# Performance work log

Hardware: AMD Instinct MI355X
Metric: run time of the kernel (lower is better)

Reference implementation:

```python
import jax, jax.numpy as jnp
import numpy as np

V_IN, V_OUT = 32000, 32000
E, H = 512, 1024
B, S, T = 64, 128, 64


def setup_inputs() -> dict:
    key = jax.random.key(0)
    ks = jax.random.split(key, 13)
    s = 0.05
    return {
        "src": jax.random.randint(ks[0], (B, S), 0, V_IN, dtype=jnp.int32),
        "trg": jax.random.randint(ks[1], (B, T), 0, V_OUT, dtype=jnp.int32),
        "tf_mask": jax.random.randint(ks[2], (T,), 0, 2, dtype=jnp.int32),
        "enc_emb": jax.random.normal(ks[3], (V_IN, E), jnp.float32) * s,
        "dec_emb": jax.random.normal(ks[4], (V_OUT, E), jnp.float32) * s,
        "Wih_e": jax.random.normal(ks[5], (4 * H, E), jnp.float32) * s,
        "Whh_e": jax.random.normal(ks[6], (4 * H, H), jnp.float32) * s,
        "b_e": jax.random.normal(ks[7], (4 * H,), jnp.float32) * s,
        "Wih_d": jax.random.normal(ks[8], (4 * H, E), jnp.float32) * s,
        "Whh_d": jax.random.normal(ks[9], (4 * H, H), jnp.float32) * s,
        "b_d": jax.random.normal(ks[10], (4 * H,), jnp.float32) * s,
        "Wfc": jax.random.normal(ks[11], (V_OUT, H), jnp.float32) * s,
        "bfc": jax.random.normal(ks[12], (V_OUT,), jnp.float32) * s,
    }


def lstm_step(h, c, x, Wih, Whh, b):
    # PyTorch LSTM gate order: input, forget, cell(g), output
    g = x @ Wih.T + h @ Whh.T + b  # [B, 4H]
    i, f, gg, o = jnp.split(g, 4, axis=-1)
    c_new = jax.nn.sigmoid(f) * c + jax.nn.sigmoid(i) * jnp.tanh(gg)
    h_new = jax.nn.sigmoid(o) * jnp.tanh(c_new)
    return h_new, c_new


def reference(src, trg, tf_mask, enc_emb, dec_emb, Wih_e, Whh_e, b_e,
              Wih_d, Whh_d, b_d, Wfc, bfc):
    b, t_len = trg.shape
    dt = Wfc.dtype
    hdim = Whh_e.shape[1]

    # ----- Encoder (dropout is identity in eval mode) -----
    x_src = enc_emb[src]  # [B, S, E]
    h0 = jnp.zeros((b, hdim), dt)
    c0 = jnp.zeros((b, hdim), dt)

    def enc_step(carry, x_t):
        h, c = carry
        h, c = lstm_step(h, c, x_t, Wih_e, Whh_e, b_e)
        return (h, c), None

    (h, c), _ = jax.lax.scan(enc_step, (h0, c0), jnp.swapaxes(x_src, 0, 1))

    # ----- Decoder loop over t = 1 .. T-1 -----
    def dec_step(carry, xs):
        h, c, inp = carry
        trg_t, tf = xs
        x = dec_emb[inp]  # [B, E]
        h, c = lstm_step(h, c, x, Wih_d, Whh_d, b_d)
        logits = h @ Wfc.T + bfc  # [B, V]
        nxt = jnp.where(tf > 0, trg_t, jnp.argmax(logits, axis=-1).astype(trg_t.dtype))
        return (h, c, nxt), logits

    xs = (jnp.swapaxes(trg, 0, 1)[1:], tf_mask[1:])
    _, logits = jax.lax.scan(dec_step, (h, c, trg[:, 0]), xs)  # [T-1, B, V]

    # outputs[:, 0, :] stays zeros, as in the original
    out = jnp.concatenate([jnp.zeros((1, b, logits.shape[-1]), logits.dtype), logits], axis=0)
    return jnp.swapaxes(out, 0, 1)  # [B, T, V]
```

## Files before the change

### kernel.cpp

```cpp
#include <hip/hip_runtime.h>
#include <math.h>

#define Hd 1024
#define Ed 512
#define Bv 64
#define Sv 128
#define Tv 64
#define Vv 32000
#define NB 256

typedef __attribute__((ext_vector_type(8))) short bf16x8;
typedef __attribute__((ext_vector_type(4))) float f32x4;
typedef unsigned long long ull;

__device__ __forceinline__ float sigf(float x){ return 1.0f/(1.0f + expf(-x)); }
__device__ __forceinline__ unsigned short f2bf(float f){
  unsigned u = __float_as_uint(f);
  return (unsigned short)((u + 0x7FFFu + ((u>>16)&1u)) >> 16);
}
__device__ __forceinline__ float bf2f(unsigned short b){ return __uint_as_float(((unsigned)b)<<16); }
__device__ __forceinline__ void split3(float v, unsigned short& s0, unsigned short& s1, unsigned short& s2){
  s0 = f2bf(v);
  float r1 = v - bf2f(s0);
  s1 = f2bf(r1);
  s2 = f2bf(r1 - bf2f(s1));
}
#define MF(A,B,C) __builtin_amdgcn_mfma_f32_16x16x32_bf16(A,B,C,0,0,0)

#define OFF_H    65536
#define H_PL     4259840L
#define OFF_WE   6455296
#define OFF_WD   15892480
#define W_PL     6291456L
#define OFF_WF   25329664
#define WF_PL    32768000L
#define OFF_TOK  58097664
#define OFF_CNT  58105728
#define NEED_FL  58106240


__global__ __launch_bounds__(256) void k_wsplit3(
    const float* __restrict__ Wih, const float* __restrict__ Whh,
    unsigned short* __restrict__ d0, unsigned short* __restrict__ d1, unsigned short* __restrict__ d2)
{
  const int n = blockIdx.x;
  const int tid = threadIdx.x;
  const int g = n >> 10, jt = (n & 1023) >> 4, nl = n & 15;
  const long base = ((long)(g*64 + jt)*48) << 9;
  #pragma unroll
  for (int i = 0; i < 6; ++i){
    int k = tid + 256*i;
    float v = (k < 512) ? Wih[(long)n*512 + k] : Whh[(long)n*1024 + (k-512)];
    int kt = k >> 5, lk = (k >> 3) & 3, ke = k & 7;
    long dst = base + ((long)kt << 9) + ((lk*16 + nl) << 3) + ke;
    unsigned short s0,s1,s2; split3(v, s0,s1,s2);
    d0[dst] = s0; d1[dst] = s1; d2[dst] = s2;
  }
}

__global__ __launch_bounds__(256) void k_wfsplit(
    const float* __restrict__ W, unsigned short* __restrict__ dhi, unsigned short* __restrict__ dlo)
{
  const int v = blockIdx.x;
  const int tid = threadIdx.x;
  const int vt = v >> 4, vl = v & 15;
  const long base = ((long)vt*32) << 9;
  #pragma unroll
  for (int i = 0; i < 4; ++i){
    int k = tid + 256*i;
    float x = W[(long)v*1024 + k];
    int kt = k >> 5, lk = (k >> 3) & 3, ke = k & 7;
    long dst = base + ((long)kt << 9) + ((lk*16 + vl) << 3) + ke;
    unsigned short h = f2bf(x);
    dhi[dst] = h;
    dlo[dst] = f2bf(x - bf2f(h));
  }
}

__device__ __forceinline__ void gbar(int* cnt, int idx){
  __syncthreads();
  if (threadIdx.x == 0){
    __hip_atomic_fetch_add(&cnt[idx], 1, __ATOMIC_RELEASE, __HIP_MEMORY_SCOPE_AGENT);
    while (__hip_atomic_load(&cnt[idx], __ATOMIC_RELAXED, __HIP_MEMORY_SCOPE_AGENT) < NB)
      __builtin_amdgcn_s_sleep(2);
    __builtin_amdgcn_fence(__ATOMIC_ACQUIRE, "workgroup");
  }
  __syncthreads();
}

template<bool DEC>
__device__ __forceinline__ void lstm_phase(
    int lb, int tid, int slot_in, int slot_out, int tj,
    const unsigned short* __restrict__ W0s, const unsigned short* __restrict__ W1s,
    const unsigned short* __restrict__ W2s, const float* __restrict__ bias,
    const int* __restrict__ tok_src, const int* __restrict__ tf,
    const float* __restrict__ emb, const ull* __restrict__ toku,
    unsigned short* __restrict__ H, float* __restrict__ c,
    float (*g4)[16][16], short (*hst)[16][16], int* stok)
{
  const bool act = (tid < 256);
  const int g = (tid >> 6) & 3, lane = tid & 63;
  const int l15 = lane & 15, lk = lane >> 4;
  const int jh = (lb & 63) * 16;
  const int m0 = (lb >> 6) * 16;
  const int mt = lb >> 6;
  const long wbase = ((long)(g*64 + (lb & 63))*48) << 9;
  const unsigned short* w0 = W0s + wbase;
  const unsigned short* w1 = W1s + wbase;
  const unsigned short* w2 = W2s + wbase;
  const unsigned short* h0 = H + (long)slot_in*65536;
  const unsigned short* h1 = h0 + H_PL;
  const unsigned short* h2 = h0 + 2*H_PL;

  if (tid < 16){
    int m = m0 + tid, tk;
    if (!DEC){
      tk = tok_src[m*Sv + tj];
    } else {
      if (tj == 0) tk = tok_src[m*Tv];
      else if (tf[tj] > 0) tk = tok_src[m*Tv + tj];
      else tk = (int)(~(unsigned)__hip_atomic_load(&toku[(long)(tj-1)*64 + m],
                     __ATOMIC_RELAXED, __HIP_MEMORY_SCOPE_AGENT));
    }
    stok[tid] = tk;
  }
  __syncthreads();

  if (act){
    f32x4 acc = (f32x4){0.f,0.f,0.f,0.f};

    {
      const float* e0 = emb + (long)stok[l15]*Ed;
      #pragma unroll 2
      for (int kt = 0; kt < 16; ++kt){
        const int k0 = kt*32 + lk*8;
        bf16x8 b0  = *(const bf16x8*)(w0 + ((long)kt << 9) + (lane << 3));
        bf16x8 b1v = *(const bf16x8*)(w1 + ((long)kt << 9) + (lane << 3));
        bf16x8 b2  = *(const bf16x8*)(w2 + ((long)kt << 9) + (lane << 3));
        bf16x8 a0,a1,a2;
        float4 pa = *(const float4*)(e0 + k0);
        float4 pb = *(const float4*)(e0 + k0 + 4);
        float fv[8] = {pa.x,pa.y,pa.z,pa.w,pb.x,pb.y,pb.z,pb.w};
        #pragma unroll
        for (int e=0;e<8;++e){ unsigned short s0,s1,s2; split3(fv[e],s0,s1,s2);
          a0[e]=(short)s0; a1[e]=(short)s1; a2[e]=(short)s2; }
        acc = MF(a0,b0,acc); acc = MF(a1,b0,acc); acc = MF(a0,b1v,acc);
        acc = MF(a2,b0,acc); acc = MF(a0,b2,acc); acc = MF(a1,b1v,acc);
      }
    }
    {
      #pragma unroll 2
      for (int kt = 0; kt < 32; ++kt){
        bf16x8 b0  = *(const bf16x8*)(w0 + ((long)(16+kt) << 9) + (lane << 3));
        bf16x8 b1v = *(const bf16x8*)(w1 + ((long)(16+kt) << 9) + (lane << 3));
        bf16x8 b2  = *(const bf16x8*)(w2 + ((long)(16+kt) << 9) + (lane << 3));
        const long ho = (((long)mt*32 + kt) << 9) + (lane << 3);
        bf16x8 a0 = *(const bf16x8*)(h0 + ho);
        bf16x8 a1 = *(const bf16x8*)(h1 + ho);
        bf16x8 a2 = *(const bf16x8*)(h2 + ho);
        acc = MF(a0,b0,acc); acc = MF(a1,b0,acc); acc = MF(a0,b1v,acc);
        acc = MF(a2,b0,acc); acc = MF(a0,b2,acc); acc = MF(a1,b1v,acc);
      }
    }

    #pragma unroll
    for (int r = 0; r < 4; ++r) g4[g][lk*4 + r][l15] = acc[r];
  }
  __syncthreads();

  if (act){
    const int mloc = tid >> 4, cl = tid & 15;
    const int col = jh + cl;
    float ig = g4[0][mloc][cl] + bias[col];
    float fg = g4[1][mloc][cl] + bias[Hd + col];
    float gg = g4[2][mloc][cl] + bias[2*Hd + col];
    float og = g4[3][mloc][cl] + bias[3*Hd + col];
    long idx = (long)(m0 + mloc)*Hd + col;
    float cv = c[idx];
    float cn = sigf(fg)*cv + sigf(ig)*tanhf(gg);
    float hn = sigf(og)*tanhf(cn);
    c[idx] = cn;
    unsigned short s0,s1,s2; split3(hn, s0,s1,s2);
    hst[0][mloc][cl] = (short)s0; hst[1][mloc][cl] = (short)s1; hst[2][mloc][cl] = (short)s2;
  }
  __syncthreads();
  if (tid < 192){
    const int p = tid >> 6, t2 = tid & 63, r = t2 >> 2, q = t2 & 3;
    ull v =
        (ull)(unsigned short)hst[p][r][q*4]
      | ((ull)(unsigned short)hst[p][r][q*4+1] << 16)
      | ((ull)(unsigned short)hst[p][r][q*4+2] << 32)
      | ((ull)(unsigned short)hst[p][r][q*4+3] << 48);
    const int kt = (lb & 63) >> 1;
    const int off16 = (jh & 16) + q*4;
    const int lkw = off16 >> 3, keb = off16 & 7;
    ull* dst = (ull*)(H + (long)p*H_PL + (long)slot_out*65536
                      + (((long)mt*32 + kt) << 9) + ((lkw*16 + r) << 3) + keb);
    __hip_atomic_store(dst, v, __ATOMIC_RELAXED, __HIP_MEMORY_SCOPE_AGENT);
  }
}

__device__ __forceinline__ void fc_phase(
    int b, int tid,
    const unsigned short* __restrict__ hhi, const unsigned short* __restrict__ hlo,
    const unsigned short* __restrict__ Wfhi, const unsigned short* __restrict__ Wflo,
    const float* __restrict__ bfc,
    ull* __restrict__ tslot, ull* amax)
{
  if (tid < 64) amax[tid] = 0ULL;
  __syncthreads();
  const int wv = tid >> 6, lane = tid & 63;
  const int l15 = lane & 15, lk = lane >> 4;
  const int vt = b*8 + wv;
  const int v0 = vt*16 + l15;

  f32x4 acc[4];
  #pragma unroll
  for (int mt=0; mt<4; ++mt) acc[mt] = (f32x4){0.f,0.f,0.f,0.f};

  #pragma unroll 2
  for (int kt = 0; kt < 32; ++kt){
    const long wo = (((long)vt*32 + kt) << 9) + (lane << 3);
    bf16x8 bh = *(const bf16x8*)(Wfhi + wo);
    bf16x8 bl = *(const bf16x8*)(Wflo + wo);
    #pragma unroll
    for (int mt=0; mt<4; ++mt){
      const long ho = (((long)mt*32 + kt) << 9) + (lane << 3);
      bf16x8 ah = *(const bf16x8*)(hhi + ho);
      bf16x8 al = *(const bf16x8*)(hlo + ho);
      acc[mt] = MF(ah, bh, acc[mt]);
      acc[mt] = MF(al, bh, acc[mt]);
      acc[mt] = MF(ah, bl, acc[mt]);
    }
  }
  float bb0 = bfc[v0];
  #pragma unroll
  for (int mt=0; mt<4; ++mt){
    #pragma unroll
    for (int r=0; r<4; ++r){
      int m = mt*16 + lk*4 + r;
      float f0 = acc[mt][r] + bb0;
      unsigned u0 = __float_as_uint(f0); u0 ^= (u0 >> 31) ? 0xFFFFFFFFu : 0x80000000u;
      ull cm = ((ull)u0 << 32) | (unsigned)(~v0);
      #pragma unroll
      for (int d=1; d<16; d<<=1){
        ull o = __shfl_xor(cm, d);
        if (o > cm) cm = o;
      }
      if (l15 == 0) atomicMax(&amax[m], cm);
    }
  }
  __syncthreads();
  if (tid < 64) atomicMax(tslot + tid, amax[tid]);
}

__global__ __launch_bounds__(512, 1) void k_mega(
    const int* __restrict__ src, const int* __restrict__ trg, const int* __restrict__ tf,
    const float* __restrict__ enc_emb, const float* __restrict__ dec_emb,
    const float* __restrict__ b_e, const float* __restrict__ b_d,
    const float* __restrict__ bfc,
    float* __restrict__ ws)
{
  __shared__ float g4[4][16][16];
  __shared__ short hst[3][16][16];
  __shared__ int stok[16];
  __shared__ ull amax[64];

  const int b = blockIdx.x, tid = threadIdx.x;
  const int lb = b;

  float* c = ws;
  unsigned short* H = (unsigned short*)(ws + OFF_H);
  const unsigned short* We0 = (const unsigned short*)(ws + OFF_WE);
  const unsigned short* We1 = We0 + W_PL;
  const unsigned short* We2 = We0 + 2*W_PL;
  const unsigned short* Wd0 = (const unsigned short*)(ws + OFF_WD);
  const unsigned short* Wd1 = Wd0 + W_PL;
  const unsigned short* Wd2 = Wd0 + 2*W_PL;
  const unsigned short* Wfhi = (const unsigned short*)(ws + OFF_WF);
  const unsigned short* Wflo = Wfhi + WF_PL;
  ull* toku = (ull*)(ws + OFF_TOK);
  int* cnt = (int*)(ws + OFF_CNT);
  int bar = 0;

  if (tid < 256){
    const int jh = (lb & 63)*16, m0 = (lb >> 6)*16;
    const int mloc = tid >> 4, cl = tid & 15;
    c[(long)(m0+mloc)*Hd + jh + cl] = 0.f;
    if (tid < 96){
      long off_ull = (long)lb*96 + tid;
      int p = (int)(off_ull >> 13);
      long q = off_ull & 8191;
      ull* dst = (ull*)(H + (long)p*H_PL + 64L*65536) + q;
      __hip_atomic_store(dst, 0ULL, __ATOMIC_RELAXED, __HIP_MEMORY_SCOPE_AGENT);
    }
  }
  gbar(cnt, bar++);

  for (int t = 0; t < Sv; ++t){
    lstm_phase<false>(lb, tid, 63 + ((t+1)&1), 63 + (t&1), t,
        We0, We1, We2, b_e, src, (const int*)0, enc_emb,
        (const ull*)0, H, c, g4, hst, stok);
    gbar(cnt, bar++);
  }
  for (int j = 0; j < Tv-1; ++j){
    lstm_phase<true>(lb, tid, (j == 0) ? 64 : (j-1), j, j,
        Wd0, Wd1, Wd2, b_d, trg, tf, dec_emb, toku, H, c, g4, hst, stok);
    gbar(cnt, bar++);
    if (j < Tv-2 && tf[j+1] == 0){
      if (b < 250){
        const unsigned short* h0 = H + (long)j*65536;
        fc_phase(b, tid, h0, h0 + H_PL, Wfhi, Wflo, bfc, toku + (long)j*64, amax);
      }
      gbar(cnt, bar++);
    }
  }
}

__global__ __launch_bounds__(256) void k_fcall(
    const unsigned short* __restrict__ Wfhi, const unsigned short* __restrict__ Wflo,
    const float* __restrict__ bfc,
    const unsigned short* __restrict__ H, float* __restrict__ out)
{
  const int tid = threadIdx.x;
  const int wv = tid >> 6, lane = tid & 63;
  const int l15 = lane & 15, lk = lane >> 4;
  const int vt = blockIdx.x*4 + wv;
  const int vcol = vt*16 + l15;
  const int jbase = blockIdx.y*4;
  const unsigned short* h0b = H + (long)jbase*65536;
  const unsigned short* h1b = h0b + H_PL;

  f32x4 acc[4][4];
  #pragma unroll
  for (int jj=0;jj<4;++jj)
    #pragma unroll
    for (int mt=0;mt<4;++mt) acc[jj][mt] = (f32x4){0.f,0.f,0.f,0.f};

  for (int kt = 0; kt < 32; ++kt){
    const long wo = (((long)vt*32 + kt) << 9) + (lane << 3);
    bf16x8 bh = *(const bf16x8*)(Wfhi + wo);
    bf16x8 bl = *(const bf16x8*)(Wflo + wo);
    #pragma unroll
    for (int jj=0;jj<4;++jj){
      if (jbase + jj <= 62){
        #pragma unroll
        for (int mt=0;mt<4;++mt){
          const long ho = (long)jj*65536 + (((long)mt*32 + kt) << 9) + (lane << 3);
          bf16x8 ah = *(const bf16x8*)(h0b + ho);
          bf16x8 al = *(const bf16x8*)(h1b + ho);
          acc[jj][mt] = MF(ah, bh, acc[jj][mt]);
          acc[jj][mt] = MF(al, bh, acc[jj][mt]);
          acc[jj][mt] = MF(ah, bl, acc[jj][mt]);
        }
      }
    }
  }
  float bb = bfc[vcol];
  #pragma unroll
  for (int jj=0;jj<4;++jj){
    if (jbase + jj <= 62){
      #pragma unroll
      for (int mt=0;mt<4;++mt){
        #pragma unroll
        for (int r=0;r<4;++r){
          int m = mt*16 + lk*4 + r;
          out[((long)m*Tv + (jbase+jj+1))*(long)Vv + vcol] = acc[jj][mt][r] + bb;
        }
      }
    }
  }
  if (blockIdx.y == 0){
    const int vb = blockIdx.x*64;
    for (int i = tid; i < 4096; i += 256){
      int m = i >> 6, v = vb + (i & 63);
      out[(long)m*Tv*(long)Vv + v] = 0.f;
    }
  }
}


__global__ __launch_bounds__(256) void k_initC(float* __restrict__ ws, float* __restrict__ out){
  long i = (long)blockIdx.x*256 + threadIdx.x;
  if (i < 262144){ ws[i] = 0.f; }
  else {
    long r = i - 262144;
    long m = r / Vv, v = r % Vv;
    out[m*Tv*(long)Vv + v] = 0.f;
  }
}

__global__ __launch_bounds__(256) void k_stepC(
    int mode, int t,
    const int* __restrict__ tok_src, const int* __restrict__ tf_mask,
    const int* __restrict__ token_buf, const float* __restrict__ emb,
    const float* __restrict__ Wih, const float* __restrict__ Whh,
    const float* __restrict__ bias,
    const float* __restrict__ h_in, const float* __restrict__ c_in,
    float* __restrict__ h_out, float* __restrict__ c_out,
    unsigned short* __restrict__ hsp_hi, unsigned short* __restrict__ hsp_lo)
{
  __shared__ __align__(16) float tile[8*1536];
  __shared__ float gbuf[4*8*32];
  __shared__ int toks[8];
  const int tid = threadIdx.x;
  const int m0 = blockIdx.y*8, jh0 = blockIdx.x*32;
  if (tid < 8){
    int m = m0 + tid; int tok;
    if (mode == 0) tok = tok_src[m*Sv + t];
    else { if (t == 0) tok = tok_src[m*Tv];
           else tok = (tf_mask[t] > 0) ? tok_src[m*Tv + t] : token_buf[m]; }
    toks[tid] = tok;
  }
  __syncthreads();
  { float4* t4 = (float4*)tile;
    #pragma unroll
    for (int r = 0; r < 12; ++r){
      int f = tid + 256*r; int row = f / 384, o = f % 384; float4 v;
      if (o < 128) v = ((const float4*)(emb + (long)toks[row]*Ed))[o];
      else         v = ((const float4*)(h_in + (long)(m0+row)*Hd))[o-128];
      t4[row*384 + o] = v; } }
  __syncthreads();
  const int g = tid >> 6, sx = tid & 63, jl = sx & 31, mg = sx >> 5;
  const int col = g*Hd + jh0 + jl;
  const float4* wx = (const float4*)(Wih + (long)col*Ed);
  const float4* wh = (const float4*)(Whh + (long)col*Hd);
  const float4* t4 = (const float4*)tile;
  const int mb = mg*4;
  float bq = bias[col];
  float a0=bq, a1=bq, a2=bq, a3=bq;
  for (int k = 0; k < 128; ++k){
    float4 w = wx[k];
    float4 v0 = t4[(mb+0)*384 + k]; float4 v1 = t4[(mb+1)*384 + k];
    float4 v2 = t4[(mb+2)*384 + k]; float4 v3 = t4[(mb+3)*384 + k];
    a0 += w.x*v0.x + w.y*v0.y + w.z*v0.z + w.w*v0.w;
    a1 += w.x*v1.x + w.y*v1.y + w.z*v1.z + w.w*v1.w;
    a2 += w.x*v2.x + w.y*v2.y + w.z*v2.z + w.w*v2.w;
    a3 += w.x*v3.x + w.y*v3.y + w.z*v3.z + w.w*v3.w;
  }
  for (int k = 0; k < 256; ++k){
    float4 w = wh[k];
    float4 v0 = t4[(mb+0)*384 + 128 + k]; float4 v1 = t4[(mb+1)*384 + 128 + k];
    float4 v2 = t4[(mb+2)*384 + 128 + k]; float4 v3 = t4[(mb+3)*384 + 128 + k];
    a0 += w.x*v0.x + w.y*v0.y + w.z*v0.z + w.w*v0.w;
    a1 += w.x*v1.x + w.y*v1.y + w.z*v1.z + w.w*v1.w;
    a2 += w.x*v2.x + w.y*v2.y + w.z*v2.z + w.w*v2.w;
    a3 += w.x*v3.x + w.y*v3.y + w.z*v3.z + w.w*v3.w;
  }
  gbuf[g*256 + (mb+0)*32 + jl] = a0; gbuf[g*256 + (mb+1)*32 + jl] = a1;
  gbuf[g*256 + (mb+2)*32 + jl] = a2; gbuf[g*256 + (mb+3)*32 + jl] = a3;
  __syncthreads();
  const int ml = tid >> 5, j2 = tid & 31;
  float ig = gbuf[0*256 + ml*32 + j2];
  float fg = gbuf[1*256 + ml*32 + j2];
  float gg = gbuf[2*256 + ml*32 + j2];
  float og = gbuf[3*256 + ml*32 + j2];
  long idx = (long)(m0+ml)*Hd + jh0 + j2;
  float cc = c_in[idx];
  float cn = sigf(fg)*cc + sigf(ig)*tanhf(gg);
  float hn = sigf(og)*tanhf(cn);
  c_out[idx] = cn; h_out[idx] = hn;
  unsigned short hh = f2bf(hn);
  hsp_hi[idx] = hh; hsp_lo[idx] = f2bf(hn - bf2f(hh));
}

__global__ __launch_bounds__(256) void k_fcC(
    int j, const unsigned short* __restrict__ hhi, const unsigned short* __restrict__ hlo,
    const float* __restrict__ Wfc, const float* __restrict__ bfc, float* __restrict__ out)
{
  const int tid = threadIdx.x;
  const int wv = tid >> 6, lane = tid & 63;
  const int l15 = lane & 15, lk = lane >> 4;
  const int vcol = blockIdx.x*64 + wv*16 + l15;
  const float* wrow = Wfc + (long)vcol*Hd;
  f32x4 acc[4];
  #pragma unroll
  for (int mt=0; mt<4; ++mt) acc[mt] = (f32x4){0.f,0.f,0.f,0.f};
  #pragma unroll 2
  for (int kt = 0; kt < 32; ++kt){
    const int k0 = kt*32 + lk*8;
    float4 wa = *(const float4*)(wrow + k0);
    float4 wb = *(const float4*)(wrow + k0 + 4);
    float wf[8] = {wa.x,wa.y,wa.z,wa.w,wb.x,wb.y,wb.z,wb.w};
    bf16x8 bh, bl;
    #pragma unroll
    for (int e=0;e<8;++e){
      unsigned short h = f2bf(wf[e]);
      bh[e] = (short)h; bl[e] = (short)f2bf(wf[e] - bf2f(h));
    }
    #pragma unroll
    for (int mt=0; mt<4; ++mt){
      const int row = mt*16 + l15;
      bf16x8 ah = *(const bf16x8*)(hhi + row*Hd + k0);
      bf16x8 al = *(const bf16x8*)(hlo + row*Hd + k0);
      acc[mt] = MF(ah, bh, acc[mt]);
      acc[mt] = MF(al, bh, acc[mt]);
      acc[mt] = MF(ah, bl, acc[mt]);
    }
  }
  float bb = bfc[vcol];
  #pragma unroll
  for (int mt=0; mt<4; ++mt)
    #pragma unroll
    for (int r=0; r<4; ++r){
      int m = mt*16 + lk*4 + r;
      out[((long)m*Tv + (j+1))*(long)Vv + vcol] = acc[mt][r] + bb;
    }
}

__global__ __launch_bounds__(256) void k_argmaxC(
    int j, const float* __restrict__ out, int* __restrict__ token_buf)
{
  __shared__ float sval[256];
  __shared__ int   sidx[256];
  const int m = blockIdx.x, tid = threadIdx.x;
  const float* base = out + ((long)m*Tv + (j+1))*(long)Vv;
  float best = -INFINITY; int bi = 0;
  for (int v = tid; v < Vv; v += 256){
    float f = base[v];
    if (f > best){ best = f; bi = v; }
  }
  sval[tid] = best; sidx[tid] = bi;
  __syncthreads();
  for (int s2 = 128; s2 > 0; s2 >>= 1){
    if (tid < s2){
      float ov = sval[tid+s2]; int oi = sidx[tid+s2];
      if (ov > sval[tid] || (ov == sval[tid] && oi < sidx[tid])){
        sval[tid] = ov; sidx[tid] = oi;
      }
    }
    __syncthreads();
  }
  if (tid == 0) token_buf[m] = sidx[0];
}

extern "C" void kernel_launch(void* const* d_in, const int* in_sizes, int n_in,
                              void* d_out, int out_size, void* d_ws, size_t ws_size,
                              hipStream_t stream)
{
  const int*   src     = (const int*)  d_in[0];
  const int*   trg     = (const int*)  d_in[1];
  const int*   tf      = (const int*)  d_in[2];
  const float* enc_emb = (const float*)d_in[3];
  const float* dec_emb = (const float*)d_in[4];
  const float* Wih_e   = (const float*)d_in[5];
  const float* Whh_e   = (const float*)d_in[6];
  const float* b_e     = (const float*)d_in[7];
  const float* Wih_d   = (const float*)d_in[8];
  const float* Whh_d   = (const float*)d_in[9];
  const float* b_d     = (const float*)d_in[10];
  const float* Wfc     = (const float*)d_in[11];
  const float* bfc     = (const float*)d_in[12];
  float* out = (float*)d_out;
  float* ws  = (float*)d_ws;

  if (ws_size >= (size_t)NEED_FL * 4ULL){
    unsigned short* We0 = (unsigned short*)(ws + OFF_WE);
    unsigned short* Wd0 = (unsigned short*)(ws + OFF_WD);
    unsigned short* Wf0 = (unsigned short*)(ws + OFF_WF);
    unsigned short* Hb  = (unsigned short*)(ws + OFF_H);

    hipMemsetAsync((void*)(ws + OFF_TOK), 0, (size_t)(NEED_FL - OFF_TOK) * 4ULL, stream);
    k_wsplit3<<<4096, 256, 0, stream>>>(Wih_e, Whh_e, We0, We0 + W_PL, We0 + 2*W_PL);
    k_wsplit3<<<4096, 256, 0, stream>>>(Wih_d, Whh_d, Wd0, Wd0 + W_PL, Wd0 + 2*W_PL);
    k_wfsplit<<<32000, 256, 0, stream>>>(Wfc, Wf0, Wf0 + WF_PL);
    k_mega<<<NB, 512, 0, stream>>>(src, trg, tf, enc_emb, dec_emb, b_e, b_d, bfc, ws);
    k_fcall<<<dim3(500, 16), 256, 0, stream>>>(Wf0, Wf0 + WF_PL, bfc, Hb, out);
  } else {
    float* hbuf[2] = { ws,            ws + 65536 };
    float* cbuf[2] = { ws + 131072,   ws + 196608 };
    int*   tokbuf  = (int*)(ws + 262144);
    unsigned short* hsp_hi = (unsigned short*)(ws + 262208);
    unsigned short* hsp_lo = (unsigned short*)(ws + 262208 + 32768);

    k_initC<<<9024, 256, 0, stream>>>(ws, out);
    int cur = 0;
    for (int t = 0; t < Sv; ++t){
      k_stepC<<<dim3(32,8), 256, 0, stream>>>(0, t, src, tf, tokbuf, enc_emb,
          Wih_e, Whh_e, b_e, hbuf[cur], cbuf[cur], hbuf[cur^1], cbuf[cur^1], hsp_hi, hsp_lo);
      cur ^= 1;
    }
    for (int j = 0; j < Tv-1; ++j){
      k_stepC<<<dim3(32,8), 256, 0, stream>>>(1, j, trg, tf, tokbuf, dec_emb,
          Wih_d, Whh_d, b_d, hbuf[cur], cbuf[cur], hbuf[cur^1], cbuf[cur^1], hsp_hi, hsp_lo);
      cur ^= 1;
      k_fcC<<<500, 256, 0, stream>>>(j, hsp_hi, hsp_lo, Wfc, bfc, out);
      if (j < Tv-2) k_argmaxC<<<64, 256, 0, stream>>>(j, out, tokbuf);
    }
  }
}
```

Before: 9.028 ms.

## Overlap next-step input projection with recurrence and use per-row-group barriers

The idle upper 256 threads of each 512-thread block now precompute the next timestep's input-embedding projection (x·Wih) into a double-buffered shared-memory array while the lower threads run the current recurrent matmul. This takes the embedding half of the gate GEMM off the serial critical path whenever the next token is known (encoder steps, and teacher-forced decoder steps). The global barrier across all 256 blocks is replaced by barriers over the 64 blocks sharing a batch-row group, since each row group's recurrence depends only on its own H rows. A full grid barrier is kept only around the argmax FC phase. This adds shared-memory use, extra counters and more complex synchronisation logic.

```diff
diff --git a/kernel.cpp b/kernel.cpp
--- a/kernel.cpp
+++ b/kernel.cpp
@@ -36,7 +36,7 @@
 #define WF_PL    32768000L
 #define OFF_TOK  58097664
 #define OFF_CNT  58105728
-#define NEED_FL  58106240
+#define NEED_FL  58106880
 
 
 __global__ __launch_bounds__(256) void k_wsplit3(
@@ -77,26 +77,66 @@
   }
 }
 
-__device__ __forceinline__ void gbar(int* cnt, int idx){
+__device__ __forceinline__ void gbarN(int* cnt, int idx, int N){
   __syncthreads();
   if (threadIdx.x == 0){
     __hip_atomic_fetch_add(&cnt[idx], 1, __ATOMIC_RELEASE, __HIP_MEMORY_SCOPE_AGENT);
-    while (__hip_atomic_load(&cnt[idx], __ATOMIC_RELAXED, __HIP_MEMORY_SCOPE_AGENT) < NB)
+    while (__hip_atomic_load(&cnt[idx], __ATOMIC_RELAXED, __HIP_MEMORY_SCOPE_AGENT) < N)
       __builtin_amdgcn_s_sleep(2);
     __builtin_amdgcn_fence(__ATOMIC_ACQUIRE, "workgroup");
   }
   __syncthreads();
+}
+
+__device__ __forceinline__ void xpre(
+    int lb, int tid, const float* __restrict__ nemb,
+    const unsigned short* __restrict__ NW0, const unsigned short* __restrict__ NW1,
+    const unsigned short* __restrict__ NW2,
+    const int* __restrict__ stok2, float (*xgd)[64][4])
+{
+  const int g2 = (tid >> 6) & 3, lane = tid & 63;
+  const int l15 = lane & 15, lk = lane >> 4;
+  const long wb = ((long)(g2*64 + (lb & 63))*48) << 9;
+  const unsigned short* w0 = NW0 + wb;
+  const unsigned short* w1 = NW1 + wb;
+  const unsigned short* w2 = NW2 + wb;
+  f32x4 acc = (f32x4){0.f,0.f,0.f,0.f};
+  const float* e0 = nemb + (long)stok2[l15]*Ed;
+  #pragma unroll 2
+  for (int kt = 0; kt < 16; ++kt){
+    const int k0 = kt*32 + lk*8;
+    bf16x8 b0  = *(const bf16x8*)(w0 + ((long)kt << 9) + (lane << 3));
+    bf16x8 b1v = *(const bf16x8*)(w1 + ((long)kt << 9) + (lane << 3));
+    bf16x8 b2  = *(const bf16x8*)(w2 + ((long)kt << 9) + (lane << 3));
+    bf16x8 a0,a1,a2;
+    float4 pa = *(const float4*)(e0 + k0);
+    float4 pb = *(const float4*)(e0 + k0 + 4);
+    float fv[8] = {pa.x,pa.y,pa.z,pa.w,pb.x,pb.y,pb.z,pb.w};
+    #pragma unroll
+    for (int e=0;e<8;++e){ unsigned short s0,s1,s2; split3(fv[e],s0,s1,s2);
+      a0[e]=(short)s0; a1[e]=(short)s1; a2[e]=(short)s2; }
+    acc = MF(a0,b0,acc); acc = MF(a1,b0,acc); acc = MF(a0,b1v,acc);
+    acc = MF(a2,b0,acc); acc = MF(a0,b2,acc); acc = MF(a1,b1v,acc);
+  }
+  #pragma unroll
+  for (int r = 0; r < 4; ++r) xgd[g2][lane][r] = acc[r];
 }
 
 template<bool DEC>
 __device__ __forceinline__ void lstm_phase(
     int lb, int tid, int slot_in, int slot_out, int tj,
+    bool hasxg, int xb,
+    int donext, const int* __restrict__ ntok, int nstride, int nidx,
+    const float* __restrict__ nemb,
+    const unsigned short* __restrict__ NW0, const unsigned short* __restrict__ NW1,
+    const unsigned short* __restrict__ NW2,
     const unsigned short* __restrict__ W0s, const unsigned short* __restrict__ W1s,
     const unsigned short* __restrict__ W2s, const float* __restrict__ bias,
     const int* __restrict__ tok_src, const int* __restrict__ tf,
     const float* __restrict__ emb, const ull* __restrict__ toku,
     unsigned short* __restrict__ H, float* __restrict__ c,
-    float (*g4)[16][16], short (*hst)[16][16], int* stok)
+    float (*g4)[16][16], short (*hst)[16][16], int* stok, int* stok2,
+    float (*xg)[4][64][4])
 {
   const bool act = (tid < 256);
   const int g = (tid >> 6) & 3, lane = tid & 63;
@@ -112,7 +152,7 @@
   const unsigned short* h1 = h0 + H_PL;
   const unsigned short* h2 = h0 + 2*H_PL;
 
-  if (tid < 16){
+  if (!hasxg && tid < 16){
     int m = m0 + tid, tk;
     if (!DEC){
       tk = tok_src[m*Sv + tj];
@@ -124,12 +164,17 @@
     }
     stok[tid] = tk;
   }
+  if (donext && tid >= 256 && tid < 272){
+    stok2[tid-256] = ntok[(m0 + (tid-256))*nstride + nidx];
+  }
   __syncthreads();
 
   if (act){
-    f32x4 acc = (f32x4){0.f,0.f,0.f,0.f};
-
-    {
+    f32x4 acc;
+    if (hasxg){
+      acc = *(const f32x4*)&xg[xb][g][lane][0];
+    } else {
+      acc = (f32x4){0.f,0.f,0.f,0.f};
       const float* e0 = emb + (long)stok[l15]*Ed;
       #pragma unroll 2
       for (int kt = 0; kt < 16; ++kt){
@@ -148,23 +193,22 @@
         acc = MF(a2,b0,acc); acc = MF(a0,b2,acc); acc = MF(a1,b1v,acc);
       }
     }
-    {
-      #pragma unroll 2
-      for (int kt = 0; kt < 32; ++kt){
-        bf16x8 b0  = *(const bf16x8*)(w0 + ((long)(16+kt) << 9) + (lane << 3));
-        bf16x8 b1v = *(const bf16x8*)(w1 + ((long)(16+kt) << 9) + (lane << 3));
-        bf16x8 b2  = *(const bf16x8*)(w2 + ((long)(16+kt) << 9) + (lane << 3));
-        const long ho = (((long)mt*32 + kt) << 9) + (lane << 3);
-        bf16x8 a0 = *(const bf16x8*)(h0 + ho);
-        bf16x8 a1 = *(const bf16x8*)(h1 + ho);
-        bf16x8 a2 = *(const bf16x8*)(h2 + ho);
-        acc = MF(a0,b0,acc); acc = MF(a1,b0,acc); acc = MF(a0,b1v,acc);
-        acc = MF(a2,b0,acc); acc = MF(a0,b2,acc); acc = MF(a1,b1v,acc);
-      }
-    }
-
+    #pragma unroll 2
+    for (int kt = 0; kt < 32; ++kt){
+      bf16x8 b0  = *(const bf16x8*)(w0 + ((long)(16+kt) << 9) + (lane << 3));
+      bf16x8 b1v = *(const bf16x8*)(w1 + ((long)(16+kt) << 9) + (lane << 3));
+      bf16x8 b2  = *(const bf16x8*)(w2 + ((long)(16+kt) << 9) + (lane << 3));
+      const long ho = (((long)mt*32 + kt) << 9) + (lane << 3);
+      bf16x8 a0 = *(const bf16x8*)(h0 + ho);
+      bf16x8 a1 = *(const bf16x8*)(h1 + ho);
+      bf16x8 a2 = *(const bf16x8*)(h2 + ho);
+      acc = MF(a0,b0,acc); acc = MF(a1,b0,acc); acc = MF(a0,b1v,acc);
+      acc = MF(a2,b0,acc); acc = MF(a0,b2,acc); acc = MF(a1,b1v,acc);
+    }
     #pragma unroll
     for (int r = 0; r < 4; ++r) g4[g][lk*4 + r][l15] = acc[r];
+  } else if (donext){
+    xpre(lb, tid, nemb, NW0, NW1, NW2, stok2, xg[xb^1]);
   }
   __syncthreads();
 
@@ -264,10 +308,13 @@
   __shared__ float g4[4][16][16];
   __shared__ short hst[3][16][16];
   __shared__ int stok[16];
+  __shared__ int stok2[16];
   __shared__ ull amax[64];
+  __shared__ __align__(16) float xg[2][4][64][4];
 
   const int b = blockIdx.x, tid = threadIdx.x;
   const int lb = b;
+  const int m0i = (lb >> 6) * 16;
 
   float* c = ws;
   unsigned short* H = (unsigned short*)(ws + OFF_H);
@@ -280,13 +327,14 @@
   const unsigned short* Wfhi = (const unsigned short*)(ws + OFF_WF);
   const unsigned short* Wflo = Wfhi + WF_PL;
   ull* toku = (ull*)(ws + OFF_TOK);
-  int* cnt = (int*)(ws + OFF_CNT);
-  int bar = 0;
+  int* fcnt = (int*)(ws + OFF_CNT);
+  int* gcnt = fcnt + 128 + (lb >> 6)*256;
+  int fbar = 0, gb = 0;
 
   if (tid < 256){
-    const int jh = (lb & 63)*16, m0 = (lb >> 6)*16;
+    const int jh = (lb & 63)*16;
     const int mloc = tid >> 4, cl = tid & 15;
-    c[(long)(m0+mloc)*Hd + jh + cl] = 0.f;
+    c[(long)(m0i+mloc)*Hd + jh + cl] = 0.f;
     if (tid < 96){
       long off_ull = (long)lb*96 + tid;
       int p = (int)(off_ull >> 13);
@@ -295,24 +343,42 @@
       __hip_atomic_store(dst, 0ULL, __ATOMIC_RELAXED, __HIP_MEMORY_SCOPE_AGENT);
     }
   }
-  gbar(cnt, bar++);
+  if (tid >= 256 && tid < 272){
+    stok2[tid-256] = src[(m0i + (tid-256))*Sv + 0];
+  }
+  __syncthreads();
+  if (tid >= 256) xpre(lb, tid, enc_emb, We0, We1, We2, stok2, xg[0]);
+  gbarN(fcnt, fbar++, NB);
 
   for (int t = 0; t < Sv; ++t){
+    const bool last = (t == Sv-1);
     lstm_phase<false>(lb, tid, 63 + ((t+1)&1), 63 + (t&1), t,
-        We0, We1, We2, b_e, src, (const int*)0, enc_emb,
-        (const ull*)0, H, c, g4, hst, stok);
-    gbar(cnt, bar++);
+        true, t & 1,
+        1, last ? trg : src, last ? Tv : Sv, last ? 0 : (t+1),
+        last ? dec_emb : enc_emb,
+        last ? Wd0 : We0, last ? Wd1 : We1, last ? Wd2 : We2,
+        We0, We1, We2, b_e, src, (const int*)0, enc_emb, (const ull*)0,
+        H, c, g4, hst, stok, stok2, xg);
+    gbarN(gcnt, gb++, 64);
   }
   for (int j = 0; j < Tv-1; ++j){
+    const int step = Sv + j;
+    const bool hx = (j == 0) || (tf[j] > 0);
+    const int dn = (j < Tv-2 && tf[j+1] > 0) ? 1 : 0;
     lstm_phase<true>(lb, tid, (j == 0) ? 64 : (j-1), j, j,
-        Wd0, Wd1, Wd2, b_d, trg, tf, dec_emb, toku, H, c, g4, hst, stok);
-    gbar(cnt, bar++);
+        hx, step & 1,
+        dn, trg, Tv, j+1, dec_emb, Wd0, Wd1, Wd2,
+        Wd0, Wd1, Wd2, b_d, trg, tf, dec_emb, toku,
+        H, c, g4, hst, stok, stok2, xg);
     if (j < Tv-2 && tf[j+1] == 0){
+      gbarN(fcnt, fbar++, NB);
       if (b < 250){
         const unsigned short* h0 = H + (long)j*65536;
         fc_phase(b, tid, h0, h0 + H_PL, Wfhi, Wflo, bfc, toku + (long)j*64, amax);
       }
-      gbar(cnt, bar++);
+      gbarN(fcnt, fbar++, NB);
+    } else {
+      gbarN(gcnt, gb++, 64);
     }
   }
 }
```

New measurement: 8.618 ms. -4.5%, faster.
